# Performance work log

Hardware: AMD Instinct MI355X
Metric: run time of the kernel (lower is better)

Reference implementation:

```python
import jax, jax.numpy as jnp
import numpy as np

B, C, D, E, ES, TOPK = 8, 4096, 1024, 16, 256, 4096

def setup_inputs() -> dict:
    key = jax.random.key(0)
    k1, k2, k3, k4 = jax.random.split(key, 4)
    x = jax.random.normal(k1, (B, C, D), dtype=jnp.float32)
    gate = jax.random.normal(k2, (C, E), dtype=jnp.float32) / np.sqrt(D)
    lin1_weight = jax.random.normal(k3, (D, E, ES), dtype=jnp.float32) / np.sqrt(D)
    lin2_weight = jax.random.normal(k4, (E, ES, D), dtype=jnp.float32) / np.sqrt(ES)
    return {"x": x, "gate": gate, "lin1_weight": lin1_weight, "lin2_weight": lin2_weight, "topk": TOPK}

def reference(x, gate, lin1_weight, lin2_weight, topk):
    b, c, d = x.shape
    e = gate.shape[1]
    n_tokens = b * c
    # faithful to original einsum: sum x over dmodel, elementwise-mult by gate[c, e]
    gate_out = jnp.einsum('bcd,ce->bce', x, gate)            # [b, c, e]
    gate_out = jnp.transpose(gate_out, (2, 0, 1)).reshape(e, n_tokens)
    gate_out = jax.nn.softmax(gate_out, axis=1)              # softmax over tokens per expert
    topk_values, topk_indices = jax.lax.top_k(gate_out, topk)  # [e, k]
    xf = x.reshape(n_tokens, d)
    flat_idx = topk_indices.reshape(-1)
    gathered = xf[flat_idx].reshape(e, topk, d)              # dispatch
    h = jax.nn.relu(jnp.einsum('ekd,des->eks', gathered, lin1_weight))
    out = jnp.einsum('eks,esd->ekd', h, lin2_weight)
    out = out * topk_values[..., None]                       # weight by gate probs
    z = jnp.zeros_like(xf).at[flat_idx].add(out.reshape(-1, d))  # scatter-add combine
    return z.reshape(b, c, d)
```

## Files before the change

kernel.cpp:

```cpp
#include <hip/hip_runtime.h>
#include <hip/hip_bf16.h>

#define BB 8
#define CC 4096
#define DD 1024
#define EE 16
#define ESS 256
#define KSEL 4096
#define NTOK (BB*CC)
#define HLS 264

typedef short bf16x8 __attribute__((ext_vector_type(8)));
typedef float f32x4 __attribute__((ext_vector_type(4)));
typedef unsigned u32x4 __attribute__((ext_vector_type(4)));

struct PickRes { unsigned tau; unsigned n_gt; unsigned n_tie; float sm; };
struct Sel1 { unsigned b; unsigned above; unsigned kth; };

__device__ __forceinline__ short f2bf(float f) {
  unsigned u = __float_as_uint(f);
  u += 0x7FFFu + ((u >> 16) & 1u);
  return (short)(u >> 16);
}
__device__ __forceinline__ float bf2f(short s) {
  return __uint_as_float(((unsigned)(unsigned short)s) << 16);
}
__device__ __forceinline__ unsigned f2key(float f) {
  unsigned u = __float_as_uint(f);
  return (u & 0x80000000u) ? ~u : (u | 0x80000000u);
}

#define ASG __attribute__((address_space(1)))
#define ASL __attribute__((address_space(3)))
__device__ __forceinline__ void gl_lds16(void* l, const void* g) {
  __builtin_amdgcn_global_load_lds((ASG const unsigned*)g, (ASL unsigned*)l, 16, 0, 0);
}

__global__ void k_logits(const float* __restrict__ x, const float* __restrict__ gate,
                         float* __restrict__ logits, short* __restrict__ xb,
                         int* __restrict__ inv) {
  int wid = threadIdx.x >> 6, lane = threadIdx.x & 63;
  int t = blockIdx.x * 4 + wid;
  const float4* xr = reinterpret_cast<const float4*>(x + (size_t)t * DD);
  short4* xw = reinterpret_cast<short4*>(xb + (size_t)t * DD);
  float s = 0.f;
#pragma unroll
  for (int i = 0; i < 4; ++i) {
    float4 v = xr[lane + 64 * i];
    s += v.x + v.y + v.z + v.w;
    short4 p;
    p.x = f2bf(v.x); p.y = f2bf(v.y); p.z = f2bf(v.z); p.w = f2bf(v.w);
    xw[lane + 64 * i] = p;
  }
#pragma unroll
  for (int off = 32; off; off >>= 1) s += __shfl_xor(s, off);
  if (lane < EE) {
    int c = t & (CC - 1);
    logits[(size_t)lane * NTOK + t] = s * gate[c * EE + lane];
    inv[(size_t)t * EE + lane] = -1;
  }
}

__global__ __launch_bounds__(1024) void k_hist(const float* __restrict__ logits,
                                               unsigned* __restrict__ ghist,
                                               float* __restrict__ separt) {
  int e = blockIdx.x & 15, seg = blockIdx.x >> 4;
  const float* L = logits + (size_t)e * NTOK + seg * 4096;
  unsigned* Hh = ghist + (size_t)e * 65536;
  int tid = threadIdx.x;
  float sl = 0.f;
#pragma unroll
  for (int i = 0; i < 4; ++i) {
    float lv = L[tid + 1024 * i];
    atomicAdd(&Hh[f2key(lv) >> 16], 1u);
    sl += expf(lv);
  }
  __shared__ float red[1024];
  red[tid] = sl; __syncthreads();
  for (int s2 = 512; s2; s2 >>= 1) {
    if (tid < s2) red[tid] += red[tid + s2];
    __syncthreads();
  }
  if (tid == 0) separt[e * 8 + seg] = red[0];
}

__global__ __launch_bounds__(1024) void k_scan64k(
    const unsigned* __restrict__ hist, const Sel1* __restrict__ s1in, int phase,
    Sel1* __restrict__ s1out, const float* __restrict__ separt,
    PickRes* __restrict__ pres) {
  int e = blockIdx.x;
  const unsigned* Hh = hist + (size_t)e * 65536;
  int tid = threadIdx.x;
  __shared__ unsigned u0[1024], u1[1024];
  __shared__ unsigned sh_b, sh_above, sh_kth;
  unsigned target = (phase == 1) ? (unsigned)KSEL : s1in[e].kth;
  unsigned cs = 0;
  for (int j = 0; j < 64; ++j) cs += Hh[tid * 64 + j];
  u0[tid] = cs; __syncthreads();
  unsigned* src = u0; unsigned* dst = u1;
  for (int d2 = 1; d2 < 1024; d2 <<= 1) {
    unsigned v = src[tid] + ((tid + d2 < 1024) ? src[tid + d2] : 0u);
    dst[tid] = v; __syncthreads();
    unsigned* tmp = src; src = dst; dst = tmp;
  }
  unsigned above = (tid < 1023) ? src[tid + 1] : 0u;
  if (above < target && target <= src[tid]) {
    unsigned cum = above;
    for (int j = 63; j >= 0; --j) {
      unsigned h = Hh[tid * 64 + j];
      if (cum + h >= target) { sh_b = (unsigned)(tid * 64 + j); sh_above = cum; sh_kth = target - cum; break; }
      cum += h;
    }
  }
  __syncthreads();
  if (tid == 0) {
    if (phase == 1) {
      Sel1 s; s.b = sh_b; s.above = sh_above; s.kth = sh_kth;
      s1out[e] = s;
    } else {
      unsigned tau = (s1in[e].b << 16) | sh_b;
      unsigned n_gt = s1in[e].above + sh_above;
      float sm = 0.f;
      for (int j = 0; j < 8; ++j) sm += separt[e * 8 + j];
      PickRes pr; pr.tau = tau; pr.n_gt = n_gt; pr.n_tie = KSEL - n_gt; pr.sm = sm;
      pres[e] = pr;
    }
  }
}

__global__ __launch_bounds__(1024) void k_refine(const float* __restrict__ logits,
                                                 const Sel1* __restrict__ s1,
                                                 unsigned* __restrict__ hist2) {
  int e = blockIdx.x & 15, seg = blockIdx.x >> 4;
  unsigned p16 = s1[e].b;
  const float* L = logits + (size_t)e * NTOK + seg * 4096;
  unsigned* Hh = hist2 + (size_t)e * 65536;
  int tid = threadIdx.x;
#pragma unroll
  for (int i = 0; i < 4; ++i) {
    unsigned key = f2key(L[tid + 1024 * i]);
    if ((key >> 16) == p16) atomicAdd(&Hh[key & 0xFFFF], 1u);
  }
}

__global__ __launch_bounds__(1024) void k_count(const float* __restrict__ logits,
                                                const PickRes* __restrict__ pres,
                                                unsigned* __restrict__ cnts) {
  int e = blockIdx.x & 15, seg = blockIdx.x >> 4;
  PickRes pr = pres[e];
  const float* L = logits + (size_t)e * NTOK + seg * 4096;
  int tid = threadIdx.x;
  unsigned pk = 0;
#pragma unroll
  for (int i = 0; i < 4; ++i) {
    unsigned key = f2key(L[tid + 1024 * i]);
    pk += (key > pr.tau) ? 0x10000u : ((key == pr.tau) ? 1u : 0u);
  }
  __shared__ unsigned red[1024];
  red[tid] = pk; __syncthreads();
  for (int s2 = 512; s2; s2 >>= 1) {
    if (tid < s2) red[tid] += red[tid + s2];
    __syncthreads();
  }
  if (tid == 0) cnts[e * 8 + seg] = red[0];
}

__global__ void k_scan(const unsigned* __restrict__ cnts, unsigned* __restrict__ bases) {
  int e = threadIdx.x;
  if (e < EE) {
    unsigned gb = 0, qb = 0;
    for (int s = 0; s < 8; ++s) {
      unsigned c = cnts[e * 8 + s];
      bases[e * 8 + s] = (gb << 16) | qb;
      gb += c >> 16; qb += c & 0xFFFFu;
    }
  }
}

__global__ __launch_bounds__(1024) void k_compact(const float* __restrict__ logits,
                                                  const PickRes* __restrict__ pres,
                                                  const unsigned* __restrict__ bases,
                                                  int* __restrict__ sel_idx,
                                                  float* __restrict__ sel_val,
                                                  int* __restrict__ inv) {
  int e = blockIdx.x & 15, seg = blockIdx.x >> 4;
  PickRes pr = pres[e];
  const float* L = logits + (size_t)e * NTOK;
  unsigned b = bases[e * 8 + seg];
  __shared__ unsigned wtg[16], wtq[16];
  __shared__ unsigned base_g, base_q;
  int tid = threadIdx.x, wid = tid >> 6, lane = tid & 63;
  if (tid == 0) { base_g = b >> 16; base_q = b & 0xFFFFu; }
  __syncthreads();
#pragma unroll 1
  for (int i = 0; i < 4; ++i) {
    int t = seg * 4096 + tid + 1024 * i;
    float lv = L[t];
    unsigned key = f2key(lv);
    bool g = key > pr.tau, q = key == pr.tau;
    unsigned long long bg = __ballot(g), bq = __ballot(q);
    unsigned long long lm = (1ull << lane) - 1ull;
    unsigned pg = __popcll(bg & lm), pq = __popcll(bq & lm);
    if (lane == 63) { wtg[wid] = pg + (g ? 1u : 0u); wtq[wid] = pq + (q ? 1u : 0u); }
    __syncthreads();
    unsigned og = base_g, oq = base_q;
    for (int w2 = 0; w2 < wid; ++w2) { og += wtg[w2]; oq += wtq[w2]; }
    unsigned slot = 0xFFFFFFFFu;
    if (g) slot = og + pg;
    else if (q) {
      unsigned r = oq + pq;
      if (r < pr.n_tie) slot = pr.n_gt + r;
    }
    if (slot != 0xFFFFFFFFu) {
      sel_idx[(size_t)e * KSEL + slot] = t;
      sel_val[(size_t)e * KSEL + slot] = expf(lv) / pr.sm;
      inv[(size_t)t * EE + e] = e * KSEL + (int)slot;
    }
    __syncthreads();
    if (tid == 0) {
      unsigned sg = 0, sq = 0;
#pragma unroll
      for (int w2 = 0; w2 < 16; ++w2) { sg += wtg[w2]; sq += wtq[w2]; }
      base_g += sg; base_q += sq;
    }
    __syncthreads();
  }
}

__global__ void k_transpose(const float* __restrict__ src, short* __restrict__ dst,
                            int R, int C) {
  __shared__ float tile[64][65];
  int c0 = blockIdx.x * 64, r0 = blockIdx.y * 64, b = blockIdx.z;
  const float* S = src + (size_t)b * R * C;
  short* Dp = dst + (size_t)b * R * C;
  int tx = threadIdx.x & 63, ty = threadIdx.x >> 6;
#pragma unroll
  for (int i = 0; i < 16; ++i) {
    int r = ty + 4 * i;
    tile[r][tx] = S[(size_t)(r0 + r) * C + c0 + tx];
  }
  __syncthreads();
#pragma unroll
  for (int i = 0; i < 16; ++i) {
    int cR = ty + 4 * i;
    Dp[(size_t)(c0 + cR) * R + r0 + tx] = f2bf(tile[tx][cR]);
  }
}

__global__ __launch_bounds__(512, 4) void k_ff(
    const short* __restrict__ xb, const short* __restrict__ W1T,
    const short* __restrict__ W2T, const int* __restrict__ sel_idx,
    const float* __restrict__ sel_val, short* __restrict__ out) {
  int bid = blockIdx.x;
  int e = (bid & 7) + ((bid >> 9) << 3);
  int m0 = ((bid >> 3) & 63) * 64;
  __shared__ short Hl[64 * HLS];
  __shared__ bf16x8 As8[64 * 8];
  __shared__ bf16x8 Bs8[256 * 8];
  int tid = threadIdx.x, lane = tid & 63, wid = tid >> 6;
  int wr = wid >> 2, wc = wid & 3;
  const int* idxE = sel_idx + (size_t)e * KSEL;
  f32x4 acc[2][4] = {};

  int rowA = tid >> 3, sA = tid & 7;
  int xk = rowA & 7;
  const short* aSrc = xb + (size_t)idxE[m0 + rowA] * DD + (sA ^ xk) * 8;
  const short* w1Base = W1T + (size_t)e * ESS * DD + (size_t)rowA * DD + (sA ^ xk) * 8;
  const short* w2Base = W2T + (size_t)e * DD * ESS + (size_t)rowA * ESS + (sA ^ xk) * 8;

  for (int kt = 0; kt < DD / 64; ++kt) {
    int kofs = kt * 64;
    gl_lds16(&As8[tid], aSrc + kofs);
#pragma unroll
    for (int j = 0; j < 4; ++j)
      gl_lds16(&Bs8[j * 512 + tid], w1Base + (size_t)(64 * j) * DD + kofs);
    __syncthreads();
    bf16x8 af[2][2];
#pragma unroll
    for (int mg = 0; mg < 2; ++mg) {
      int row = wr * 32 + mg * 16 + (lane & 15);
#pragma unroll
      for (int h = 0; h < 2; ++h) {
        int seg = h * 4 + (lane >> 4);
        af[mg][h] = As8[row * 8 + (seg ^ (row & 7))];
      }
    }
#pragma unroll
    for (int ng = 0; ng < 4; ++ng) {
      int rowb = wc * 64 + ng * 16 + (lane & 15);
      bf16x8 b0 = Bs8[rowb * 8 + (((lane >> 4) + 0) ^ (rowb & 7))];
      bf16x8 b1 = Bs8[rowb * 8 + (((lane >> 4) + 4) ^ (rowb & 7))];
#pragma unroll
      for (int mg = 0; mg < 2; ++mg) {
        acc[mg][ng] = __builtin_amdgcn_mfma_f32_16x16x32_bf16(af[mg][0], b0, acc[mg][ng], 0, 0, 0);
        acc[mg][ng] = __builtin_amdgcn_mfma_f32_16x16x32_bf16(af[mg][1], b1, acc[mg][ng], 0, 0, 0);
      }
    }
    __syncthreads();
  }
#pragma unroll
  for (int mg = 0; mg < 2; ++mg) {
#pragma unroll
    for (int r = 0; r < 4; ++r) {
      int hrow = wr * 32 + mg * 16 + (lane >> 4) * 4 + r;
      float v = sel_val[(size_t)e * KSEL + m0 + hrow];
#pragma unroll
      for (int ng = 0; ng < 4; ++ng) {
        int col = wc * 64 + ng * 16 + (lane & 15);
        Hl[hrow * HLS + col] = f2bf(fmaxf(acc[mg][ng][r], 0.f) * v);
      }
    }
  }
  __syncthreads();
#pragma unroll 1
  for (int np = 0; np < 4; ++np) {
    int n0 = np * 256;
    f32x4 acc2[2][4] = {};
#pragma unroll 1
    for (int kt = 0; kt < ESS / 64; ++kt) {
      int kofs = kt * 64;
#pragma unroll
      for (int j = 0; j < 4; ++j)
        gl_lds16(&Bs8[j * 512 + tid], w2Base + (size_t)(n0 + 64 * j) * ESS + kofs);
      __syncthreads();
      bf16x8 af[2][2];
#pragma unroll
      for (int mg = 0; mg < 2; ++mg) {
        int row = wr * 32 + mg * 16 + (lane & 15);
#pragma unroll
        for (int h = 0; h < 2; ++h) {
          int s8 = h * 4 + (lane >> 4);
          af[mg][h] = *reinterpret_cast<const bf16x8*>(&Hl[row * HLS + kt * 64 + s8 * 8]);
        }
      }
#pragma unroll
      for (int ng = 0; ng < 4; ++ng) {
        int rowb = wc * 64 + ng * 16 + (lane & 15);
        bf16x8 b0 = Bs8[rowb * 8 + (((lane >> 4) + 0) ^ (rowb & 7))];
        bf16x8 b1 = Bs8[rowb * 8 + (((lane >> 4) + 4) ^ (rowb & 7))];
#pragma unroll
        for (int mg = 0; mg < 2; ++mg) {
          acc2[mg][ng] = __builtin_amdgcn_mfma_f32_16x16x32_bf16(af[mg][0], b0, acc2[mg][ng], 0, 0, 0);
          acc2[mg][ng] = __builtin_amdgcn_mfma_f32_16x16x32_bf16(af[mg][1], b1, acc2[mg][ng], 0, 0, 0);
        }
      }
      __syncthreads();
    }
#pragma unroll
    for (int mg = 0; mg < 2; ++mg) {
#pragma unroll
      for (int r = 0; r < 4; ++r) {
        int ml = wr * 32 + mg * 16 + (lane >> 4) * 4 + r;
        short* orow = out + ((size_t)(e * KSEL + m0 + ml)) * DD + n0 + wc * 64 + (lane & 15);
#pragma unroll
        for (int ng = 0; ng < 4; ++ng) orow[ng * 16] = f2bf(acc2[mg][ng][r]);
      }
    }
  }
}

__global__ __launch_bounds__(512, 4) void k_gemm1(
    const short* __restrict__ xb, const short* __restrict__ W1T,
    const int* __restrict__ sel_idx, const float* __restrict__ sel_val,
    short* __restrict__ H) {
  int bid = blockIdx.x;
  int m0 = ((bid >> 3) & 31) * 128;
  int e = (bid & 7) + ((bid >> 8) << 3);
  __shared__ bf16x8 As8[128 * 8];
  __shared__ bf16x8 Bs8[256 * 8];
  int tid = threadIdx.x, lane = tid & 63, wid = tid >> 6;
  int wr = wid >> 2, wc = wid & 3;
  const int* idxE = sel_idx + (size_t)e * KSEL;
  f32x4 acc[4][4] = {};

  int rowA = tid >> 3, sA = tid & 7;
  int xk = rowA & 7;
  const short* aSrc0 = xb + (size_t)idxE[m0 + rowA] * DD + (sA ^ xk) * 8;
  const short* aSrc1 = xb + (size_t)idxE[m0 + rowA + 64] * DD + (sA ^ xk) * 8;
  const short* wBase = W1T + (size_t)e * ESS * DD + (size_t)rowA * DD + (sA ^ xk) * 8;

  for (int kt = 0; kt < DD / 64; ++kt) {
    int kofs = kt * 64;
    gl_lds16(&As8[tid], aSrc0 + kofs);
    gl_lds16(&As8[512 + tid], aSrc1 + kofs);
#pragma unroll
    for (int j = 0; j < 4; ++j)
      gl_lds16(&Bs8[j * 512 + tid], wBase + (size_t)(64 * j) * DD + kofs);
    __syncthreads();
    bf16x8 af[4][2];
#pragma unroll
    for (int mg = 0; mg < 4; ++mg) {
      int row = wr * 64 + mg * 16 + (lane & 15);
#pragma unroll
      for (int h = 0; h < 2; ++h) {
        int seg = h * 4 + (lane >> 4);
        af[mg][h] = As8[row * 8 + (seg ^ (row & 7))];
      }
    }
#pragma unroll
    for (int ng = 0; ng < 4; ++ng) {
      int rowb = wc * 64 + ng * 16 + (lane & 15);
      bf16x8 b0 = Bs8[rowb * 8 + (((lane >> 4) + 0) ^ (rowb & 7))];
      bf16x8 b1 = Bs8[rowb * 8 + (((lane >> 4) + 4) ^ (rowb & 7))];
#pragma unroll
      for (int mg = 0; mg < 4; ++mg) {
        acc[mg][ng] = __builtin_amdgcn_mfma_f32_16x16x32_bf16(af[mg][0], b0, acc[mg][ng], 0, 0, 0);
        acc[mg][ng] = __builtin_amdgcn_mfma_f32_16x16x32_bf16(af[mg][1], b1, acc[mg][ng], 0, 0, 0);
      }
    }
    __syncthreads();
  }
#pragma unroll
  for (int mg = 0; mg < 4; ++mg) {
#pragma unroll
    for (int r = 0; r < 4; ++r) {
      int ml = wr * 64 + mg * 16 + (lane >> 4) * 4 + r;
      float v = sel_val[(size_t)e * KSEL + m0 + ml];
      short* hrow = H + ((size_t)(e * KSEL + m0 + ml)) * ESS + wc * 64 + (lane & 15);
#pragma unroll
      for (int ng = 0; ng < 4; ++ng) {
        float o = fmaxf(acc[mg][ng][r], 0.f) * v;
        hrow[ng * 16] = f2bf(o);
      }
    }
  }
}

__global__ __launch_bounds__(512, 4) void k_gemm2_atomic(
    const short* __restrict__ H, const short* __restrict__ W2T,
    const int* __restrict__ sel_idx, float* __restrict__ z) {
  int bid = blockIdx.x;
  int p = (bid & 7) + ((bid >> 8) << 3);
  int m0 = ((bid >> 3) & 31) * 128;
  int n0 = (p & 3) * 256;
  int e = p >> 2;
  __shared__ bf16x8 As8[128 * 8];
  __shared__ bf16x8 Bs8[256 * 8];
  int tid = threadIdx.x, lane = tid & 63, wid = tid >> 6;
  int wr = wid >> 2, wc = wid & 3;
  f32x4 acc[4][4] = {};

  int rowA = tid >> 3, sA = tid & 7;
  int xk = rowA & 7;
  const short* hBase = H + (size_t)(e * KSEL + m0 + rowA) * ESS + (sA ^ xk) * 8;
  const short* w2Base = W2T + (size_t)(e * DD + n0 + rowA) * ESS + (sA ^ xk) * 8;

  for (int kt = 0; kt < ESS / 64; ++kt) {
    int kofs = kt * 64;
    gl_lds16(&As8[tid], hBase + kofs);
    gl_lds16(&As8[512 + tid], hBase + (size_t)64 * ESS + kofs);
#pragma unroll
    for (int j = 0; j < 4; ++j)
      gl_lds16(&Bs8[j * 512 + tid], w2Base + (size_t)(64 * j) * ESS + kofs);
    __syncthreads();
    bf16x8 af[4][2];
#pragma unroll
    for (int mg = 0; mg < 4; ++mg) {
      int row = wr * 64 + mg * 16 + (lane & 15);
#pragma unroll
      for (int h = 0; h < 2; ++h) {
        int seg = h * 4 + (lane >> 4);
        af[mg][h] = As8[row * 8 + (seg ^ (row & 7))];
      }
    }
#pragma unroll
    for (int ng = 0; ng < 4; ++ng) {
      int rowb = wc * 64 + ng * 16 + (lane & 15);
      bf16x8 b0 = Bs8[rowb * 8 + (((lane >> 4) + 0) ^ (rowb & 7))];
      bf16x8 b1 = Bs8[rowb * 8 + (((lane >> 4) + 4) ^ (rowb & 7))];
#pragma unroll
      for (int mg = 0; mg < 4; ++mg) {
        acc[mg][ng] = __builtin_amdgcn_mfma_f32_16x16x32_bf16(af[mg][0], b0, acc[mg][ng], 0, 0, 0);
        acc[mg][ng] = __builtin_amdgcn_mfma_f32_16x16x32_bf16(af[mg][1], b1, acc[mg][ng], 0, 0, 0);
      }
    }
    __syncthreads();
  }
#pragma unroll
  for (int mg = 0; mg < 4; ++mg) {
#pragma unroll
    for (int r = 0; r < 4; ++r) {
      int ml = wr * 64 + mg * 16 + (lane >> 4) * 4 + r;
      int token = sel_idx[(size_t)e * KSEL + m0 + ml];
      float* zr = z + (size_t)token * DD + n0 + wc * 64 + (lane & 15);
#pragma unroll
      for (int ng = 0; ng < 4; ++ng) atomicAdd(zr + ng * 16, acc[mg][ng][r]);
    }
  }
}

__global__ __launch_bounds__(256) void k_combine(const short* __restrict__ out,
                                                 const int* __restrict__ inv,
                                                 float* __restrict__ z) {
  int wid = threadIdx.x >> 6, lane = threadIdx.x & 63;
  int tA = (blockIdx.x * 4 + wid) * 2;
  int tB = tA + 1;
  int gA[16], gB[16];
  const int4* ivA = reinterpret_cast<const int4*>(inv + (size_t)tA * EE);
  const int4* ivB = reinterpret_cast<const int4*>(inv + (size_t)tB * EE);
#pragma unroll
  for (int q = 0; q < 4; ++q) {
    int4 va = ivA[q];
    gA[4 * q] = va.x; gA[4 * q + 1] = va.y; gA[4 * q + 2] = va.z; gA[4 * q + 3] = va.w;
    int4 vb = ivB[q];
    gB[4 * q] = vb.x; gB[4 * q + 1] = vb.y; gB[4 * q + 2] = vb.z; gB[4 * q + 3] = vb.w;
  }
  float accA[16] = {}, accB[16] = {};
#pragma unroll
  for (int e = 0; e < EE; ++e) {
    if (gA[e] >= 0) {
      const u32x4* rp = reinterpret_cast<const u32x4*>(out + (size_t)gA[e] * DD + lane * 16);
      u32x4 v0 = rp[0], v1 = rp[1];
      const short* s0 = reinterpret_cast<const short*>(&v0);
      const short* s1 = reinterpret_cast<const short*>(&v1);
#pragma unroll
      for (int i = 0; i < 8; ++i) accA[i] += bf2f(s0[i]);
#pragma unroll
      for (int i = 0; i < 8; ++i) accA[8 + i] += bf2f(s1[i]);
    }
    if (gB[e] >= 0) {
      const u32x4* rp = reinterpret_cast<const u32x4*>(out + (size_t)gB[e] * DD + lane * 16);
      u32x4 v0 = rp[0], v1 = rp[1];
      const short* s0 = reinterpret_cast<const short*>(&v0);
      const short* s1 = reinterpret_cast<const short*>(&v1);
#pragma unroll
      for (int i = 0; i < 8; ++i) accB[i] += bf2f(s0[i]);
#pragma unroll
      for (int i = 0; i < 8; ++i) accB[8 + i] += bf2f(s1[i]);
    }
  }
  float4* zwA = reinterpret_cast<float4*>(z + (size_t)tA * DD + lane * 16);
  float4* zwB = reinterpret_cast<float4*>(z + (size_t)tB * DD + lane * 16);
#pragma unroll
  for (int i = 0; i < 4; ++i) {
    float4 oa;
    oa.x = accA[4 * i]; oa.y = accA[4 * i + 1]; oa.z = accA[4 * i + 2]; oa.w = accA[4 * i + 3];
    zwA[i] = oa;
    float4 ob;
    ob.x = accB[4 * i]; ob.y = accB[4 * i + 1]; ob.z = accB[4 * i + 2]; ob.w = accB[4 * i + 3];
    zwB[i] = ob;
  }
}

extern "C" void kernel_launch(void* const* d_in, const int* in_sizes, int n_in,
                              void* d_out, int out_size, void* d_ws, size_t ws_size,
                              hipStream_t stream) {
  (void)in_sizes; (void)n_in;
  const float* x = (const float*)d_in[0];
  const float* gate = (const float*)d_in[1];
  const float* lin1 = (const float*)d_in[2];
  const float* lin2 = (const float*)d_in[3];
  float* z = (float*)d_out;

  char* ws = (char*)d_ws;
  size_t off = 0;
  auto alloc = [&](size_t bytes) -> void* {
    off = (off + 255) & ~(size_t)255;
    void* p = ws + off;
    off += bytes;
    return p;
  };
  float* logits = (float*)alloc((size_t)EE * NTOK * 4);
  int* sidx = (int*)alloc((size_t)EE * KSEL * 4);
  float* sval = (float*)alloc((size_t)EE * KSEL * 4);
  int* inv = (int*)alloc((size_t)NTOK * EE * 4);
  short* W1T = (short*)alloc((size_t)EE * ESS * DD * 2);
  short* W2T = (short*)alloc((size_t)EE * DD * ESS * 2);
  short* H = (short*)alloc((size_t)EE * KSEL * ESS * 2);
  short* xb = (short*)alloc((size_t)NTOK * DD * 2);
  size_t out_bytes = (size_t)EE * KSEL * DD * 2;
  bool combine = (off + 256 + out_bytes) <= ws_size;
  short* outbuf = combine ? (short*)alloc(out_bytes) : nullptr;

  unsigned* ghist = (unsigned*)H;
  unsigned* hist2 = (unsigned*)((char*)H + (size_t)4 * 1024 * 1024);
  float* separt = (float*)((char*)H + (size_t)8 * 1024 * 1024);
  Sel1* s1 = (Sel1*)((char*)separt + 1024);
  PickRes* pres = (PickRes*)((char*)s1 + 1024);
  unsigned* cnts = (unsigned*)((char*)pres + 1024);
  unsigned* bases = (unsigned*)((char*)cnts + 1024);

  k_transpose<<<dim3(64, 16, 1), 256, 0, stream>>>(lin1, W1T, DD, EE * ESS);
  k_transpose<<<dim3(16, 4, 16), 256, 0, stream>>>(lin2, W2T, ESS, DD);
  k_logits<<<NTOK / 4, 256, 0, stream>>>(x, gate, logits, xb, inv);
  hipMemsetAsync(ghist, 0, (size_t)8 * 1024 * 1024, stream);
  k_hist<<<128, 1024, 0, stream>>>(logits, ghist, separt);
  k_scan64k<<<EE, 1024, 0, stream>>>(ghist, s1, 1, s1, separt, pres);
  k_refine<<<128, 1024, 0, stream>>>(logits, s1, hist2);
  k_scan64k<<<EE, 1024, 0, stream>>>(hist2, s1, 2, s1, separt, pres);
  k_count<<<128, 1024, 0, stream>>>(logits, pres, cnts);
  k_scan<<<1, 64, 0, stream>>>(cnts, bases);
  k_compact<<<128, 1024, 0, stream>>>(logits, pres, bases, sidx, sval, inv);
  if (combine) {
    k_ff<<<1024, 512, 0, stream>>>(xb, W1T, W2T, sidx, sval, outbuf);
    k_combine<<<NTOK / 8, 256, 0, stream>>>(outbuf, inv, z);
  } else {
    hipMemsetAsync(d_out, 0, (size_t)out_size * sizeof(float), stream);
    k_gemm1<<<512, 512, 0, stream>>>(xb, W1T, sidx, sval, H);
    k_gemm2_atomic<<<2048, 512, 0, stream>>>(H, W2T, sidx, z);
  }
}
```

Baseline: 313.9 us.

## Enlarge FF tile to 128 rows, prefetch W2 tiles, fuse count/scan into compact

The fused FFN kernel now handles 128 selected tokens per block instead of 64, with each wave computing a 32x128 output tile, so W1/W2 tile loads are reused across twice as many rows. The second GEMM is flattened into one 16-step loop that issues the next W2 tile load after the current MFMAs, and the H tile in LDS is XOR-swizzled to reduce bank conflicts. The separate count and scan kernels are removed: each compact block recounts all preceding segments itself, which saves two launches but adds redundant reads of the logits. The combine kernel now handles four tokens per wave, and occupancy bounds drop to 2 blocks per CU.

Measured after the change: 344.4 us. 9.7% more time.

```diff
diff --git a/kernel.cpp b/kernel.cpp
--- a/kernel.cpp
+++ b/kernel.cpp
@@ -143,55 +143,33 @@
   }
 }
 
-__global__ __launch_bounds__(1024) void k_count(const float* __restrict__ logits,
-                                                const PickRes* __restrict__ pres,
-                                                unsigned* __restrict__ cnts) {
-  int e = blockIdx.x & 15, seg = blockIdx.x >> 4;
-  PickRes pr = pres[e];
-  const float* L = logits + (size_t)e * NTOK + seg * 4096;
-  int tid = threadIdx.x;
-  unsigned pk = 0;
-#pragma unroll
-  for (int i = 0; i < 4; ++i) {
-    unsigned key = f2key(L[tid + 1024 * i]);
-    pk += (key > pr.tau) ? 0x10000u : ((key == pr.tau) ? 1u : 0u);
-  }
-  __shared__ unsigned red[1024];
-  red[tid] = pk; __syncthreads();
-  for (int s2 = 512; s2; s2 >>= 1) {
-    if (tid < s2) red[tid] += red[tid + s2];
-    __syncthreads();
-  }
-  if (tid == 0) cnts[e * 8 + seg] = red[0];
-}
-
-__global__ void k_scan(const unsigned* __restrict__ cnts, unsigned* __restrict__ bases) {
-  int e = threadIdx.x;
-  if (e < EE) {
-    unsigned gb = 0, qb = 0;
-    for (int s = 0; s < 8; ++s) {
-      unsigned c = cnts[e * 8 + s];
-      bases[e * 8 + s] = (gb << 16) | qb;
-      gb += c >> 16; qb += c & 0xFFFFu;
-    }
-  }
-}
-
 __global__ __launch_bounds__(1024) void k_compact(const float* __restrict__ logits,
                                                   const PickRes* __restrict__ pres,
-                                                  const unsigned* __restrict__ bases,
                                                   int* __restrict__ sel_idx,
                                                   float* __restrict__ sel_val,
                                                   int* __restrict__ inv) {
   int e = blockIdx.x & 15, seg = blockIdx.x >> 4;
   PickRes pr = pres[e];
   const float* L = logits + (size_t)e * NTOK;
-  unsigned b = bases[e * 8 + seg];
+  __shared__ unsigned redg[1024], redq[1024];
   __shared__ unsigned wtg[16], wtq[16];
   __shared__ unsigned base_g, base_q;
   int tid = threadIdx.x, wid = tid >> 6, lane = tid & 63;
-  if (tid == 0) { base_g = b >> 16; base_q = b & 0xFFFFu; }
+
+  unsigned cg = 0, cq = 0;
+  for (int t = tid; t < seg * 4096; t += 1024) {
+    unsigned key = f2key(L[t]);
+    cg += (key > pr.tau) ? 1u : 0u;
+    cq += (key == pr.tau) ? 1u : 0u;
+  }
+  redg[tid] = cg; redq[tid] = cq; __syncthreads();
+  for (int s2 = 512; s2; s2 >>= 1) {
+    if (tid < s2) { redg[tid] += redg[tid + s2]; redq[tid] += redq[tid + s2]; }
+    __syncthreads();
+  }
+  if (tid == 0) { base_g = redg[0]; base_q = redq[0]; }
   __syncthreads();
+
 #pragma unroll 1
   for (int i = 0; i < 4; ++i) {
     int t = seg * 4096 + tid + 1024 * i;
@@ -247,30 +225,32 @@
   }
 }
 
-__global__ __launch_bounds__(512, 4) void k_ff(
+__global__ __launch_bounds__(512, 2) void k_ff(
     const short* __restrict__ xb, const short* __restrict__ W1T,
     const short* __restrict__ W2T, const int* __restrict__ sel_idx,
     const float* __restrict__ sel_val, short* __restrict__ out) {
   int bid = blockIdx.x;
-  int e = (bid & 7) + ((bid >> 9) << 3);
-  int m0 = ((bid >> 3) & 63) * 64;
-  __shared__ short Hl[64 * HLS];
-  __shared__ bf16x8 As8[64 * 8];
+  int e = (bid & 7) + ((bid >> 8) << 3);
+  int m0 = ((bid >> 3) & 31) * 128;
+  __shared__ short Hl[128 * HLS];
+  __shared__ bf16x8 As8[128 * 8];
   __shared__ bf16x8 Bs8[256 * 8];
   int tid = threadIdx.x, lane = tid & 63, wid = tid >> 6;
-  int wr = wid >> 2, wc = wid & 3;
+  int wr = wid >> 1, wc = wid & 1;
   const int* idxE = sel_idx + (size_t)e * KSEL;
-  f32x4 acc[2][4] = {};
+  f32x4 acc[2][8] = {};
 
   int rowA = tid >> 3, sA = tid & 7;
   int xk = rowA & 7;
-  const short* aSrc = xb + (size_t)idxE[m0 + rowA] * DD + (sA ^ xk) * 8;
+  const short* aSrc0 = xb + (size_t)idxE[m0 + rowA] * DD + (sA ^ xk) * 8;
+  const short* aSrc1 = xb + (size_t)idxE[m0 + rowA + 64] * DD + (sA ^ xk) * 8;
   const short* w1Base = W1T + (size_t)e * ESS * DD + (size_t)rowA * DD + (sA ^ xk) * 8;
   const short* w2Base = W2T + (size_t)e * DD * ESS + (size_t)rowA * ESS + (sA ^ xk) * 8;
 
   for (int kt = 0; kt < DD / 64; ++kt) {
     int kofs = kt * 64;
-    gl_lds16(&As8[tid], aSrc + kofs);
+    gl_lds16(&As8[tid], aSrc0 + kofs);
+    gl_lds16(&As8[512 + tid], aSrc1 + kofs);
 #pragma unroll
     for (int j = 0; j < 4; ++j)
       gl_lds16(&Bs8[j * 512 + tid], w1Base + (size_t)(64 * j) * DD + kofs);
@@ -286,8 +266,8 @@
       }
     }
 #pragma unroll
-    for (int ng = 0; ng < 4; ++ng) {
-      int rowb = wc * 64 + ng * 16 + (lane & 15);
+    for (int ng = 0; ng < 8; ++ng) {
+      int rowb = wc * 128 + ng * 16 + (lane & 15);
       bf16x8 b0 = Bs8[rowb * 8 + (((lane >> 4) + 0) ^ (rowb & 7))];
       bf16x8 b1 = Bs8[rowb * 8 + (((lane >> 4) + 4) ^ (rowb & 7))];
 #pragma unroll
@@ -299,63 +279,81 @@
     __syncthreads();
   }
 #pragma unroll
+  for (int j = 0; j < 4; ++j)
+    gl_lds16(&Bs8[j * 512 + tid], w2Base + (size_t)(64 * j) * ESS);
+#pragma unroll
   for (int mg = 0; mg < 2; ++mg) {
 #pragma unroll
     for (int r = 0; r < 4; ++r) {
       int hrow = wr * 32 + mg * 16 + (lane >> 4) * 4 + r;
       float v = sel_val[(size_t)e * KSEL + m0 + hrow];
-#pragma unroll
-      for (int ng = 0; ng < 4; ++ng) {
-        int col = wc * 64 + ng * 16 + (lane & 15);
-        Hl[hrow * HLS + col] = f2bf(fmaxf(acc[mg][ng][r], 0.f) * v);
+      int rx = ((hrow >> 2) & 3) << 4;
+#pragma unroll
+      for (int ng = 0; ng < 8; ++ng) {
+        int col = wc * 128 + ng * 16 + (lane & 15);
+        Hl[hrow * HLS + (col ^ rx)] = f2bf(fmaxf(acc[mg][ng][r], 0.f) * v);
       }
     }
   }
   __syncthreads();
+  f32x4 acc2[2][8] = {};
 #pragma unroll 1
-  for (int np = 0; np < 4; ++np) {
-    int n0 = np * 256;
-    f32x4 acc2[2][4] = {};
-#pragma unroll 1
-    for (int kt = 0; kt < ESS / 64; ++kt) {
-      int kofs = kt * 64;
+  for (int s = 0; s < 16; ++s) {
+    int kt = s & 3;
+    bf16x8 af[2][2];
+#pragma unroll
+    for (int mg = 0; mg < 2; ++mg) {
+      int row = wr * 32 + mg * 16 + (lane & 15);
+      int rx = ((row >> 2) & 3) << 4;
+#pragma unroll
+      for (int h = 0; h < 2; ++h) {
+        int s8 = h * 4 + (lane >> 4);
+        int colx = (kt * 64 + s8 * 8) ^ rx;
+        af[mg][h] = *reinterpret_cast<const bf16x8*>(&Hl[row * HLS + colx]);
+      }
+    }
+#pragma unroll
+    for (int ng = 0; ng < 8; ++ng) {
+      int rowb = wc * 128 + ng * 16 + (lane & 15);
+      bf16x8 b0 = Bs8[rowb * 8 + (((lane >> 4) + 0) ^ (rowb & 7))];
+      bf16x8 b1 = Bs8[rowb * 8 + (((lane >> 4) + 4) ^ (rowb & 7))];
+#pragma unroll
+      for (int mg = 0; mg < 2; ++mg) {
+        acc2[mg][ng] = __builtin_amdgcn_mfma_f32_16x16x32_bf16(af[mg][0], b0, acc2[mg][ng], 0, 0, 0);
+        acc2[mg][ng] = __builtin_amdgcn_mfma_f32_16x16x32_bf16(af[mg][1], b1, acc2[mg][ng], 0, 0, 0);
+      }
+    }
+    __syncthreads();
+    if (s < 15) {
+      int s2 = s + 1;
+      int np2 = s2 >> 2, kt2 = s2 & 3;
 #pragma unroll
       for (int j = 0; j < 4; ++j)
-        gl_lds16(&Bs8[j * 512 + tid], w2Base + (size_t)(n0 + 64 * j) * ESS + kofs);
-      __syncthreads();
-      bf16x8 af[2][2];
+        gl_lds16(&Bs8[j * 512 + tid],
+                 w2Base + (size_t)(np2 * 256 + 64 * j) * ESS + kt2 * 64);
+    }
+    if (kt == 3) {
+      int np = s >> 2;
+      int n0 = np * 256;
 #pragma unroll
       for (int mg = 0; mg < 2; ++mg) {
-        int row = wr * 32 + mg * 16 + (lane & 15);
-#pragma unroll
-        for (int h = 0; h < 2; ++h) {
-          int s8 = h * 4 + (lane >> 4);
-          af[mg][h] = *reinterpret_cast<const bf16x8*>(&Hl[row * HLS + kt * 64 + s8 * 8]);
+#pragma unroll
+        for (int r = 0; r < 4; ++r) {
+          int ml = wr * 32 + mg * 16 + (lane >> 4) * 4 + r;
+          short* orow = out + ((size_t)(e * KSEL + m0 + ml)) * DD + n0 + wc * 128 + (lane & 15);
+#pragma unroll
+          for (int ng = 0; ng < 8; ++ng) orow[ng * 16] = f2bf(acc2[mg][ng][r]);
         }
       }
 #pragma unroll
-      for (int ng = 0; ng < 4; ++ng) {
-        int rowb = wc * 64 + ng * 16 + (lane & 15);
-        bf16x8 b0 = Bs8[rowb * 8 + (((lane >> 4) + 0) ^ (rowb & 7))];
-        bf16x8 b1 = Bs8[rowb * 8 + (((lane >> 4) + 4) ^ (rowb & 7))];
-#pragma unroll
-        for (int mg = 0; mg < 2; ++mg) {
-          acc2[mg][ng] = __builtin_amdgcn_mfma_f32_16x16x32_bf16(af[mg][0], b0, acc2[mg][ng], 0, 0, 0);
-          acc2[mg][ng] = __builtin_amdgcn_mfma_f32_16x16x32_bf16(af[mg][1], b1, acc2[mg][ng], 0, 0, 0);
+      for (int mg = 0; mg < 2; ++mg)
+#pragma unroll
+        for (int ng = 0; ng < 8; ++ng) {
+          f32x4 zz = {0.f, 0.f, 0.f, 0.f};
+          acc2[mg][ng] = zz;
         }
-      }
-      __syncthreads();
-    }
-#pragma unroll
-    for (int mg = 0; mg < 2; ++mg) {
-#pragma unroll
-      for (int r = 0; r < 4; ++r) {
-        int ml = wr * 32 + mg * 16 + (lane >> 4) * 4 + r;
-        short* orow = out + ((size_t)(e * KSEL + m0 + ml)) * DD + n0 + wc * 64 + (lane & 15);
-#pragma unroll
-        for (int ng = 0; ng < 4; ++ng) orow[ng * 16] = f2bf(acc2[mg][ng][r]);
-      }
-    }
+    }
+    if (s < 15) __syncthreads();
   }
 }
 
@@ -493,19 +491,18 @@
                                                  const int* __restrict__ inv,
                                                  float* __restrict__ z) {
   int wid = threadIdx.x >> 6, lane = threadIdx.x & 63;
-  int tA = (blockIdx.x * 4 + wid) * 2;
-  int tB = tA + 1;
-  int gA[16], gB[16];
-  const int4* ivA = reinterpret_cast<const int4*>(inv + (size_t)tA * EE);
-  const int4* ivB = reinterpret_cast<const int4*>(inv + (size_t)tB * EE);
+  int tA = (blockIdx.x * 4 + wid) * 4;
+  int gA[16], gB[16], gC[16], gD[16];
+  const int4* iv = reinterpret_cast<const int4*>(inv + (size_t)tA * EE);
 #pragma unroll
   for (int q = 0; q < 4; ++q) {
-    int4 va = ivA[q];
-    gA[4 * q] = va.x; gA[4 * q + 1] = va.y; gA[4 * q + 2] = va.z; gA[4 * q + 3] = va.w;
-    int4 vb = ivB[q];
-    gB[4 * q] = vb.x; gB[4 * q + 1] = vb.y; gB[4 * q + 2] = vb.z; gB[4 * q + 3] = vb.w;
-  }
-  float accA[16] = {}, accB[16] = {};
+    int4 v0 = iv[q], v1 = iv[4 + q], v2 = iv[8 + q], v3 = iv[12 + q];
+    gA[4 * q] = v0.x; gA[4 * q + 1] = v0.y; gA[4 * q + 2] = v0.z; gA[4 * q + 3] = v0.w;
+    gB[4 * q] = v1.x; gB[4 * q + 1] = v1.y; gB[4 * q + 2] = v1.z; gB[4 * q + 3] = v1.w;
+    gC[4 * q] = v2.x; gC[4 * q + 1] = v2.y; gC[4 * q + 2] = v2.z; gC[4 * q + 3] = v2.w;
+    gD[4 * q] = v3.x; gD[4 * q + 1] = v3.y; gD[4 * q + 2] = v3.z; gD[4 * q + 3] = v3.w;
+  }
+  float accA[16] = {}, accB[16] = {}, accC[16] = {}, accD[16] = {};
 #pragma unroll
   for (int e = 0; e < EE; ++e) {
     if (gA[e] >= 0) {
@@ -514,9 +511,7 @@
       const short* s0 = reinterpret_cast<const short*>(&v0);
       const short* s1 = reinterpret_cast<const short*>(&v1);
 #pragma unroll
-      for (int i = 0; i < 8; ++i) accA[i] += bf2f(s0[i]);
-#pragma unroll
-      for (int i = 0; i < 8; ++i) accA[8 + i] += bf2f(s1[i]);
+      for (int i = 0; i < 8; ++i) { accA[i] += bf2f(s0[i]); accA[8 + i] += bf2f(s1[i]); }
     }
     if (gB[e] >= 0) {
       const u32x4* rp = reinterpret_cast<const u32x4*>(out + (size_t)gB[e] * DD + lane * 16);
@@ -524,21 +519,40 @@
       const short* s0 = reinterpret_cast<const short*>(&v0);
       const short* s1 = reinterpret_cast<const short*>(&v1);
 #pragma unroll
-      for (int i = 0; i < 8; ++i) accB[i] += bf2f(s0[i]);
-#pragma unroll
-      for (int i = 0; i < 8; ++i) accB[8 + i] += bf2f(s1[i]);
+      for (int i = 0; i < 8; ++i) { accB[i] += bf2f(s0[i]); accB[8 + i] += bf2f(s1[i]); }
+    }
+    if (gC[e] >= 0) {
+      const u32x4* rp = reinterpret_cast<const u32x4*>(out + (size_t)gC[e] * DD + lane * 16);
+      u32x4 v0 = rp[0], v1 = rp[1];
+      const short* s0 = reinterpret_cast<const short*>(&v0);
+      const short* s1 = reinterpret_cast<const short*>(&v1);
+#pragma unroll
+      for (int i = 0; i < 8; ++i) { accC[i] += bf2f(s0[i]); accC[8 + i] += bf2f(s1[i]); }
+    }
+    if (gD[e] >= 0) {
+      const u32x4* rp = reinterpret_cast<const u32x4*>(out + (size_t)gD[e] * DD + lane * 16);
+      u32x4 v0 = rp[0], v1 = rp[1];
+      const short* s0 = reinterpret_cast<const short*>(&v0);
+      const short* s1 = reinterpret_cast<const short*>(&v1);
+#pragma unroll
+      for (int i = 0; i < 8; ++i) { accD[i] += bf2f(s0[i]); accD[8 + i] += bf2f(s1[i]); }
     }
   }
   float4* zwA = reinterpret_cast<float4*>(z + (size_t)tA * DD + lane * 16);
-  float4* zwB = reinterpret_cast<float4*>(z + (size_t)tB * DD + lane * 16);
+  float4* zwB = reinterpret_cast<float4*>(z + (size_t)(tA + 1) * DD + lane * 16);
+  float4* zwC = reinterpret_cast<float4*>(z + (size_t)(tA + 2) * DD + lane * 16);
+  float4* zwD = reinterpret_cast<float4*>(z + (size_t)(tA + 3) * DD + lane * 16);
 #pragma unroll
   for (int i = 0; i < 4; ++i) {
-    float4 oa;
-    oa.x = accA[4 * i]; oa.y = accA[4 * i + 1]; oa.z = accA[4 * i + 2]; oa.w = accA[4 * i + 3];
-    zwA[i] = oa;
-    float4 ob;
-    ob.x = accB[4 * i]; ob.y = accB[4 * i + 1]; ob.z = accB[4 * i + 2]; ob.w = accB[4 * i + 3];
-    zwB[i] = ob;
+    float4 o;
+    o.x = accA[4 * i]; o.y = accA[4 * i + 1]; o.z = accA[4 * i + 2]; o.w = accA[4 * i + 3];
+    zwA[i] = o;
+    o.x = accB[4 * i]; o.y = accB[4 * i + 1]; o.z = accB[4 * i + 2]; o.w = accB[4 * i + 3];
+    zwB[i] = o;
+    o.x = accC[4 * i]; o.y = accC[4 * i + 1]; o.z = accC[4 * i + 2]; o.w = accC[4 * i + 3];
+    zwC[i] = o;
+    o.x = accD[4 * i]; o.y = accD[4 * i + 1]; o.z = accD[4 * i + 2]; o.w = accD[4 * i + 3];
+    zwD[i] = o;
   }
 }
 
@@ -577,8 +591,6 @@
   float* separt = (float*)((char*)H + (size_t)8 * 1024 * 1024);
   Sel1* s1 = (Sel1*)((char*)separt + 1024);
   PickRes* pres = (PickRes*)((char*)s1 + 1024);
-  unsigned* cnts = (unsigned*)((char*)pres + 1024);
-  unsigned* bases = (unsigned*)((char*)cnts + 1024);
 
   k_transpose<<<dim3(64, 16, 1), 256, 0, stream>>>(lin1, W1T, DD, EE * ESS);
   k_transpose<<<dim3(16, 4, 16), 256, 0, stream>>>(lin2, W2T, ESS, DD);
@@ -588,12 +600,10 @@
   k_scan64k<<<EE, 1024, 0, stream>>>(ghist, s1, 1, s1, separt, pres);
   k_refine<<<128, 1024, 0, stream>>>(logits, s1, hist2);
   k_scan64k<<<EE, 1024, 0, stream>>>(hist2, s1, 2, s1, separt, pres);
-  k_count<<<128, 1024, 0, stream>>>(logits, pres, cnts);
-  k_scan<<<1, 64, 0, stream>>>(cnts, bases);
-  k_compact<<<128, 1024, 0, stream>>>(logits, pres, bases, sidx, sval, inv);
+  k_compact<<<128, 1024, 0, stream>>>(logits, pres, sidx, sval, inv);
   if (combine) {
-    k_ff<<<1024, 512, 0, stream>>>(xb, W1T, W2T, sidx, sval, outbuf);
-    k_combine<<<NTOK / 8, 256, 0, stream>>>(outbuf, inv, z);
+    k_ff<<<512, 512, 0, stream>>>(xb, W1T, W2T, sidx, sval, outbuf);
+    k_combine<<<NTOK / 16, 256, 0, stream>>>(outbuf, inv, z);
   } else {
     hipMemsetAsync(d_out, 0, (size_t)out_size * sizeof(float), stream);
     k_gemm1<<<512, 512, 0, stream>>>(xb, W1T, sidx, sval, H);
```
